# Performance work log

Measured on AMD Instinct MI355X. Metric: run time of the kernel, lower is better.

## Reference

```python
import jax, jax.numpy as jnp
import numpy as np

U1 = 512
U2 = 512
BATCH = 8192
INPUT_DIM = (U1 + U2) * 3  # 3072
UNITS = U2 * 3             # 1536


def _build_mask():
    """Replicates the block-structured random 0/1 unit_diags construction.

    Unit blocks (rows): [0,U2), [U2,2U2), [2U2,3U2).
    Input blocks (cols): ds1,ds2,ds3 of width U1 each, then stn1,stn2,stn3 of width U2.
    Each (unit-block, input-block) pair has a fixed Bernoulli keep-probability
    derived from the original randint(2)/randint(4) logic.
    """
    rng = np.random.default_rng(0)
    col_edges = [0, U1, 2 * U1, 3 * U1, 3 * U1 + U2, 3 * U1 + 2 * U2, 3 * U1 + 3 * U2]
    # keep-probabilities per unit-block (rows) x input-block (cols)
    probs = [
        [1.0, 0.5, 0.0, 1.0, 0.5, 0.0],   # units [0, U2)
        [0.5, 0.75, 0.5, 0.5, 0.75, 0.5], # units [U2, 2U2): randint(4)>0 -> p=0.75
        [0.0, 0.5, 1.0, 0.0, 0.5, 1.0],   # units [2U2, 3U2)
    ]
    p = np.zeros((UNITS, INPUT_DIM), dtype=np.float32)
    for ub in range(3):
        for j in range(6):
            p[ub * U2:(ub + 1) * U2, col_edges[j]:col_edges[j + 1]] = probs[ub][j]
    mask = (rng.random((UNITS, INPUT_DIM)) < p).astype(np.float32)
    return mask


def setup_inputs() -> dict:
    key = jax.random.key(0)
    k1, k2 = jax.random.split(key)
    x = jax.random.normal(k1, (BATCH, INPUT_DIM), dtype=jnp.float32)
    # w_init = uniform(0, 0.01), non-negative constrained
    w = jax.random.uniform(k2, (INPUT_DIM, UNITS), dtype=jnp.float32, minval=0.0, maxval=0.01)
    # gpi_bias = [0, 0] -> bias initialized to zeros
    b = jnp.zeros((UNITS,), dtype=jnp.float32)
    mask = jnp.asarray(_build_mask())  # (UNITS, INPUT_DIM), fixed 0/1 constants
    return {"x": x, "w": w, "b": b, "mask": mask}


def reference(x, w, b, mask):
    # Original: p[b,u,:] = mask[u,:] * x[b,:] ;  f = diag_part(p @ w) + b
    # => f[b,u] = sum_i mask[u,i] * x[b,i] * w[i,u] + b[u]
    # Collapses to a masked linear: x @ (mask.T * w) + b
    return x @ (mask.T * w) + b
```

## Files before the change

kernel.cpp:

```cpp
#include <hip/hip_runtime.h>
#include <stdint.h>

#define MDIM 8192
#define NDIM 1536
#define KDIM 3072

#define BM 128
#define BN 128
#define BK 96

#define NMB ((KDIM / 64) * (NDIM / 64))
#define NCVT ((MDIM * KDIM / 4) / 256)

typedef unsigned short u16;
typedef float  f32x4  __attribute__((ext_vector_type(4)));
typedef __bf16 bf16x8 __attribute__((ext_vector_type(8)));

__device__ __forceinline__ u16 f2bf(float f) {
    union { float f; unsigned int u; } v; v.f = f;
    unsigned int u = v.u;
    return (u16)((u + 0x7fffu + ((u >> 16) & 1u)) >> 16);
}

__global__ void prep_kernel(const float* __restrict__ w, const float* __restrict__ mask,
                            u16* __restrict__ Bt,
                            const float4* __restrict__ x, ushort4* __restrict__ xb) {
    const int t = threadIdx.x;
    if (blockIdx.x < NMB) {
        __shared__ float sw[64][65];
        const int kb = blockIdx.x % (KDIM / 64);
        const int nb = blockIdx.x / (KDIM / 64);
        const int k0 = kb * 64, n0 = nb * 64;
        {
            const int c4 = t & 15;
            const int r  = t >> 4;
#pragma unroll
            for (int rr = 0; rr < 4; ++rr) {
                int row = rr * 16 + r;
                float4 v = *(const float4*)&w[(size_t)(k0 + row) * NDIM + n0 + c4 * 4];
                sw[row][c4 * 4 + 0] = v.x;
                sw[row][c4 * 4 + 1] = v.y;
                sw[row][c4 * 4 + 2] = v.z;
                sw[row][c4 * 4 + 3] = v.w;
            }
        }
        __syncthreads();
        {
            const int n  = t >> 2;
            const int ks = (t & 3) * 16;
#pragma unroll
            for (int j = 0; j < 4; ++j) {
                int k = ks + j * 4;
                float4 mv = *(const float4*)&mask[(size_t)(n0 + n) * KDIM + k0 + k];
                ushort4 o;
                o.x = f2bf(mv.x * sw[k + 0][n]);
                o.y = f2bf(mv.y * sw[k + 1][n]);
                o.z = f2bf(mv.z * sw[k + 2][n]);
                o.w = f2bf(mv.w * sw[k + 3][n]);
                *(ushort4*)&Bt[(size_t)(n0 + n) * KDIM + k0 + k] = o;
            }
        }
    } else {
        int i = (blockIdx.x - NMB) * 256 + t;
        float4 v = x[i];
        ushort4 o;
        o.x = f2bf(v.x); o.y = f2bf(v.y); o.z = f2bf(v.z); o.w = f2bf(v.w);
        xb[i] = o;
    }
}

__device__ __forceinline__ void gload_lds16(const void* g, void* l) {
    __builtin_amdgcn_global_load_lds(
        (const __attribute__((address_space(1))) unsigned int*)g,
        (__attribute__((address_space(3))) unsigned int*)l, 16, 0, 0);
}

#define PLANE 4096

__global__ void __launch_bounds__(256, 3)
gemm_kernel(const u16* __restrict__ A,
            const u16* __restrict__ B,
            const float* __restrict__ bias,
            float* __restrict__ C) {
    __shared__ u16 sA[3 * PLANE];
    __shared__ u16 sB[3 * PLANE];

    const int tid  = threadIdx.x;
    const int wave = tid >> 6;
    const int lane = tid & 63;

    const int bik = blockIdx.x;
    const int by  = (bik & 7) * 8 + ((bik >> 3) & 7);
    const int bx  = bik >> 6;
    const int m0 = by * BM, n0 = bx * BN;

    const int srow = lane >> 2;
    const int scol = ((lane & 3) ^ ((lane >> 3) & 3)) * 8;

    const int wm = (wave >> 1) * 64;
    const int wn = (wave & 1) * 64;
    const int fr = lane & 15;
    const int fq = lane >> 4;
    const int fsw = (fq ^ ((fr >> 1) & 3)) * 8;

    f32x4 acc[4][4] = {};

    const u16* gA0 = A + (size_t)(m0 + wave * 16 + srow) * KDIM + scol;
    const u16* gB0 = B + (size_t)(n0 + wave * 16 + srow) * KDIM + scol;
    u16* lA0 = &sA[(wave * 16) * 32];
    u16* lA1 = &sA[(wave * 16 + 64) * 32];
    u16* lB0 = &sB[(wave * 16) * 32];
    u16* lB1 = &sB[(wave * 16 + 64) * 32];

    for (int k0 = 0; k0 < KDIM; k0 += BK) {
        __syncthreads();
#pragma unroll
        for (int p = 0; p < 3; ++p) {
            gload_lds16(gA0 + k0 + p * 32,                      lA0 + p * PLANE);
            gload_lds16(gA0 + k0 + p * 32 + (size_t)64 * KDIM,  lA1 + p * PLANE);
            gload_lds16(gB0 + k0 + p * 32,                      lB0 + p * PLANE);
            gload_lds16(gB0 + k0 + p * 32 + (size_t)64 * KDIM,  lB1 + p * PLANE);
        }
        __syncthreads();

#pragma unroll
        for (int h = 0; h < 3; ++h) {
            const u16* pA = &sA[h * PLANE];
            const u16* pB = &sB[h * PLANE];
            bf16x8 af[4], bfv[4];
#pragma unroll
            for (int mt = 0; mt < 4; ++mt)
                af[mt] = *(const bf16x8*)&pA[(wm + mt * 16 + fr) * 32 + fsw];
#pragma unroll
            for (int nt = 0; nt < 4; ++nt)
                bfv[nt] = *(const bf16x8*)&pB[(wn + nt * 16 + fr) * 32 + fsw];
#pragma unroll
            for (int mt = 0; mt < 4; ++mt)
#pragma unroll
                for (int nt = 0; nt < 4; ++nt)
                    acc[mt][nt] = __builtin_amdgcn_mfma_f32_16x16x32_bf16(
                        af[mt], bfv[nt], acc[mt][nt], 0, 0, 0);
        }
    }

#pragma unroll
    for (int nt = 0; nt < 4; ++nt) {
        int n = n0 + wn + nt * 16 + fr;
        float bv = bias[n];
#pragma unroll
        for (int mt = 0; mt < 4; ++mt) {
            int m = m0 + wm + mt * 16 + fq * 4;
#pragma unroll
            for (int r = 0; r < 4; ++r)
                C[(size_t)(m + r) * NDIM + n] = acc[mt][nt][r] + bv;
        }
    }
}

extern "C" void kernel_launch(void* const* d_in, const int* in_sizes, int n_in,
                              void* d_out, int out_size, void* d_ws, size_t ws_size,
                              hipStream_t stream) {
    const float* x    = (const float*)d_in[0];
    const float* w    = (const float*)d_in[1];
    const float* bias = (const float*)d_in[2];
    const float* mask = (const float*)d_in[3];
    float* out = (float*)d_out;

    u16* xb = (u16*)d_ws;
    u16* Bt = (u16*)((char*)d_ws + (size_t)50331648);

    prep_kernel<<<NMB + NCVT, 256, 0, stream>>>(w, mask, Bt, (const float4*)x, (ushort4*)xb);
    gemm_kernel<<<(MDIM / BM) * (NDIM / BN), 256, 0, stream>>>(xb, Bt, bias, out);
}
```

Measured before the change: 281.6 us.

## Fuse x fp32-to-bf16 conversion into GEMM A-tile loads with register prefetch

Removes the separate pass that converted x to bf16 in workspace. The GEMM now reads fp32 x directly into registers, converts to bf16 and stores into the swizzled LDS tile, prefetching the next K-slice's x into registers while the MFMAs run. This drops a full write and re-read of the bf16 copy of x. In exchange, each GEMM block reads fp32 A (twice the bytes of bf16) from global memory once per N tile, and the prefetch buffer adds register pressure under launch bounds of 3 blocks per CU.

```diff
diff --git a/kernel.cpp b/kernel.cpp
--- a/kernel.cpp
+++ b/kernel.cpp
@@ -10,7 +10,6 @@
 #define BK 96
 
 #define NMB ((KDIM / 64) * (NDIM / 64))
-#define NCVT ((MDIM * KDIM / 4) / 256)
 
 typedef unsigned short u16;
 typedef float  f32x4  __attribute__((ext_vector_type(4)));
@@ -23,49 +22,40 @@
 }
 
 __global__ void prep_kernel(const float* __restrict__ w, const float* __restrict__ mask,
-                            u16* __restrict__ Bt,
-                            const float4* __restrict__ x, ushort4* __restrict__ xb) {
+                            u16* __restrict__ Bt) {
     const int t = threadIdx.x;
-    if (blockIdx.x < NMB) {
-        __shared__ float sw[64][65];
-        const int kb = blockIdx.x % (KDIM / 64);
-        const int nb = blockIdx.x / (KDIM / 64);
-        const int k0 = kb * 64, n0 = nb * 64;
-        {
-            const int c4 = t & 15;
-            const int r  = t >> 4;
+    __shared__ float sw[64][65];
+    const int kb = blockIdx.x % (KDIM / 64);
+    const int nb = blockIdx.x / (KDIM / 64);
+    const int k0 = kb * 64, n0 = nb * 64;
+    {
+        const int c4 = t & 15;
+        const int r  = t >> 4;
 #pragma unroll
-            for (int rr = 0; rr < 4; ++rr) {
-                int row = rr * 16 + r;
-                float4 v = *(const float4*)&w[(size_t)(k0 + row) * NDIM + n0 + c4 * 4];
-                sw[row][c4 * 4 + 0] = v.x;
-                sw[row][c4 * 4 + 1] = v.y;
-                sw[row][c4 * 4 + 2] = v.z;
-                sw[row][c4 * 4 + 3] = v.w;
-            }
+        for (int rr = 0; rr < 4; ++rr) {
+            int row = rr * 16 + r;
+            float4 v = *(const float4*)&w[(size_t)(k0 + row) * NDIM + n0 + c4 * 4];
+            sw[row][c4 * 4 + 0] = v.x;
+            sw[row][c4 * 4 + 1] = v.y;
+            sw[row][c4 * 4 + 2] = v.z;
+            sw[row][c4 * 4 + 3] = v.w;
         }
-        __syncthreads();
-        {
-            const int n  = t >> 2;
-            const int ks = (t & 3) * 16;
+    }
+    __syncthreads();
+    {
+        const int n  = t >> 2;
+        const int ks = (t & 3) * 16;
 #pragma unroll
-            for (int j = 0; j < 4; ++j) {
-                int k = ks + j * 4;
-                float4 mv = *(const float4*)&mask[(size_t)(n0 + n) * KDIM + k0 + k];
-                ushort4 o;
-                o.x = f2bf(mv.x * sw[k + 0][n]);
-                o.y = f2bf(mv.y * sw[k + 1][n]);
-                o.z = f2bf(mv.z * sw[k + 2][n]);
-                o.w = f2bf(mv.w * sw[k + 3][n]);
-                *(ushort4*)&Bt[(size_t)(n0 + n) * KDIM + k0 + k] = o;
-            }
+        for (int j = 0; j < 4; ++j) {
+            int k = ks + j * 4;
+            float4 mv = *(const float4*)&mask[(size_t)(n0 + n) * KDIM + k0 + k];
+            ushort4 o;
+            o.x = f2bf(mv.x * sw[k + 0][n]);
+            o.y = f2bf(mv.y * sw[k + 1][n]);
+            o.z = f2bf(mv.z * sw[k + 2][n]);
+            o.w = f2bf(mv.w * sw[k + 3][n]);
+            *(ushort4*)&Bt[(size_t)(n0 + n) * KDIM + k0 + k] = o;
         }
-    } else {
-        int i = (blockIdx.x - NMB) * 256 + t;
-        float4 v = x[i];
-        ushort4 o;
-        o.x = f2bf(v.x); o.y = f2bf(v.y); o.z = f2bf(v.z); o.w = f2bf(v.w);
-        xb[i] = o;
     }
 }
 
@@ -78,7 +68,7 @@
 #define PLANE 4096
 
 __global__ void __launch_bounds__(256, 3)
-gemm_kernel(const u16* __restrict__ A,
+gemm_kernel(const float* __restrict__ X,
             const u16* __restrict__ B,
             const float* __restrict__ bias,
             float* __restrict__ C) {
@@ -95,7 +85,15 @@
     const int m0 = by * BM, n0 = bx * BN;
 
     const int srow = lane >> 2;
-    const int scol = ((lane & 3) ^ ((lane >> 3) & 3)) * 8;
+    const int gc   = (lane & 3) ^ ((lane >> 3) & 3);
+
+    const u16* gB0 = B + (size_t)(n0 + wave * 16 + srow) * KDIM + gc * 8;
+    u16* lB0 = &sB[(wave * 16) * 32];
+    u16* lB1 = &sB[(wave * 16 + 64) * 32];
+
+    const float* gXlo = X + (size_t)(m0 + wave * 16 + srow) * KDIM + gc * 8;
+    const float* gXhi = gXlo + (size_t)64 * KDIM;
+    u16* lA = &sA[(wave * 16 + srow) * 32 + (lane & 3) * 8];
 
     const int wm = (wave >> 1) * 64;
     const int wn = (wave & 1) * 64;
@@ -104,24 +102,48 @@
     const int fsw = (fq ^ ((fr >> 1) & 3)) * 8;
 
     f32x4 acc[4][4] = {};
+    f32x4 pa[12];
 
-    const u16* gA0 = A + (size_t)(m0 + wave * 16 + srow) * KDIM + scol;
-    const u16* gB0 = B + (size_t)(n0 + wave * 16 + srow) * KDIM + scol;
-    u16* lA0 = &sA[(wave * 16) * 32];
-    u16* lA1 = &sA[(wave * 16 + 64) * 32];
-    u16* lB0 = &sB[(wave * 16) * 32];
-    u16* lB1 = &sB[(wave * 16 + 64) * 32];
+#pragma unroll
+    for (int p = 0; p < 3; ++p) {
+        pa[4 * p + 0] = *(const f32x4*)(gXlo + p * 32);
+        pa[4 * p + 1] = *(const f32x4*)(gXlo + p * 32 + 4);
+        pa[4 * p + 2] = *(const f32x4*)(gXhi + p * 32);
+        pa[4 * p + 3] = *(const f32x4*)(gXhi + p * 32 + 4);
+    }
 
     for (int k0 = 0; k0 < KDIM; k0 += BK) {
         __syncthreads();
 #pragma unroll
         for (int p = 0; p < 3; ++p) {
-            gload_lds16(gA0 + k0 + p * 32,                      lA0 + p * PLANE);
-            gload_lds16(gA0 + k0 + p * 32 + (size_t)64 * KDIM,  lA1 + p * PLANE);
             gload_lds16(gB0 + k0 + p * 32,                      lB0 + p * PLANE);
             gload_lds16(gB0 + k0 + p * 32 + (size_t)64 * KDIM,  lB1 + p * PLANE);
         }
+#pragma unroll
+        for (int p = 0; p < 3; ++p) {
+            bf16x8 lo, hi;
+#pragma unroll
+            for (int i = 0; i < 4; ++i) {
+                lo[i]     = (__bf16)pa[4 * p + 0][i];
+                lo[i + 4] = (__bf16)pa[4 * p + 1][i];
+                hi[i]     = (__bf16)pa[4 * p + 2][i];
+                hi[i + 4] = (__bf16)pa[4 * p + 3][i];
+            }
+            *(bf16x8*)(lA + p * PLANE)           = lo;
+            *(bf16x8*)(lA + p * PLANE + 64 * 32) = hi;
+        }
         __syncthreads();
+
+        const int kn = k0 + BK;
+        if (kn < KDIM) {
+#pragma unroll
+            for (int p = 0; p < 3; ++p) {
+                pa[4 * p + 0] = *(const f32x4*)(gXlo + kn + p * 32);
+                pa[4 * p + 1] = *(const f32x4*)(gXlo + kn + p * 32 + 4);
+                pa[4 * p + 2] = *(const f32x4*)(gXhi + kn + p * 32);
+                pa[4 * p + 3] = *(const f32x4*)(gXhi + kn + p * 32 + 4);
+            }
+        }
 
 #pragma unroll
         for (int h = 0; h < 3; ++h) {
@@ -166,9 +188,8 @@
     const float* mask = (const float*)d_in[3];
     float* out = (float*)d_out;
 
-    u16* xb = (u16*)d_ws;
-    u16* Bt = (u16*)((char*)d_ws + (size_t)50331648);
+    u16* Bt = (u16*)d_ws;
 
-    prep_kernel<<<NMB + NCVT, 256, 0, stream>>>(w, mask, Bt, (const float4*)x, (ushort4*)xb);
-    gemm_kernel<<<(MDIM / BM) * (NDIM / BN), 256, 0, stream>>>(xb, Bt, bias, out);
+    prep_kernel<<<NMB, 256, 0, stream>>>(w, mask, Bt);
+    gemm_kernel<<<(MDIM / BM) * (NDIM / BN), 256, 0, stream>>>(x, Bt, bias, out);
 }
```

After: 292.6 us. 1.04x slower.
